# Performance work log

Hardware: AMD Instinct MI355X
Metric: run time of the kernel (lower is better)

Reference implementation:

```python
import jax, jax.numpy as jnp
import numpy as np
from jax import lax

POS_CANDIDATE = 128
SCL_TEMP = 0.1
BASE_SCL_TEMP = 0.07
N = 4096  # args.batch_size == total feature rows
D = 256
NUM_CLASSES = 8


def setup_inputs() -> dict:
    key = jax.random.key(0)
    k1, k2 = jax.random.split(key)
    features = jax.random.normal(k1, (N, D), dtype=jnp.float32)
    labels = jax.random.randint(k2, (N // 2,), 0, NUM_CLASSES, dtype=jnp.int64)
    return {"features": features, "labels": labels, "n_views": 1}


def reference(features, labels, n_views):
    n = features.shape[0]
    # labels path: mask_{ij} = 1 if same class
    lab = jnp.concatenate([labels, labels], axis=0).reshape(-1, 1)  # [N,1]
    mask = (lab == lab.T).astype(jnp.float32)                       # [N,N]

    # L2 normalize rows
    f = features / jnp.linalg.norm(features, axis=1, keepdims=True)

    # pairwise euclidean distances on detached features
    fd = lax.stop_gradient(f)
    sq = jnp.sum(fd * fd, axis=1)                                   # [N]
    d2 = sq[:, None] + sq[None, :] - 2.0 * (fd @ fd.T)
    dist = jnp.sqrt(jnp.maximum(d2, 0.0))                           # [N,N]

    # torch.topk default largest=True -> farthest POS_CANDIDATE indices
    _, pos_idx = lax.top_k(dist, POS_CANDIDATE)                     # [N,K]
    rows = jnp.arange(n)[:, None]
    dist_mask = jnp.zeros((n, n), jnp.float32).at[rows, pos_idx].set(1.0)

    # contrastive logits
    anchor_dot_contrast = (f @ f.T) / SCL_TEMP
    logits_max = jnp.max(anchor_dot_contrast, axis=1, keepdims=True)
    logits = anchor_dot_contrast - lax.stop_gradient(logits_max)

    # zero out self-contrast (arange scatter == zero diagonal, n_views=1)
    logits_mask = 1.0 - jnp.eye(n, dtype=jnp.float32)
    mask = mask * logits_mask

    exp_logits = jnp.exp(logits) * logits_mask
    log_prob = logits - jnp.log(jnp.sum(exp_logits, axis=1, keepdims=True))

    final_mask = mask * dist_mask
    mean_log_prob_pos = jnp.sum(final_mask * log_prob, axis=1) / jnp.sum(final_mask, axis=1)

    loss = -(SCL_TEMP / BASE_SCL_TEMP) * mean_log_prob_pos
    return jnp.mean(loss.reshape(n_views, n))
```

## Files before the change

### kernel.cpp

```cpp
#include <hip/hip_runtime.h>
#include <hip/hip_bf16.h>
#include <math.h>

#define NROWS 4096
#define DIM   256
#define HALF_MASK 2047
#define BLOCK 256

typedef __attribute__((ext_vector_type(8))) short bf16x8;
typedef __attribute__((ext_vector_type(4))) float f32x4;

__device__ __forceinline__ unsigned fkey(float f) {
    unsigned u = __float_as_uint(f);
    return (u & 0x80000000u) ? ~u : (u | 0x80000000u);
}

__device__ __forceinline__ unsigned qkey(float dot) {
    const float f = fmaf(dot, -2147483648.f, 2147483648.f);
    return (unsigned)fminf(fmaxf(f, 0.f), 4294967040.f);
}

__device__ __forceinline__ float bf16f(unsigned short b) {
    return __uint_as_float(((unsigned)b) << 16);
}


__global__ void prep_bf16_kernel(const float* __restrict__ feat,
                                 const int* __restrict__ labels,
                                 short* __restrict__ fnb,
                                 float* __restrict__ sq,
                                 unsigned char* __restrict__ lab8)
{
    const int row  = blockIdx.x * 4 + (threadIdx.x >> 6);
    const int lane = threadIdx.x & 63;
    float4 x = ((const float4*)feat)[(size_t)row * 64 + lane];
    float ss = x.x*x.x + x.y*x.y + x.z*x.z + x.w*x.w;
    #pragma unroll
    for (int m = 1; m < 64; m <<= 1) ss += __shfl_xor(ss, m, 64);
    const float nrm = sqrtf(ss);
    float4 f; f.x = x.x/nrm; f.y = x.y/nrm; f.z = x.z/nrm; f.w = x.w/nrm;

    union { __hip_bfloat16 b; unsigned short s; } cv[4];
    cv[0].b = __float2bfloat16(f.x); cv[1].b = __float2bfloat16(f.y);
    cv[2].b = __float2bfloat16(f.z); cv[3].b = __float2bfloat16(f.w);
    ushort4 h; h.x = cv[0].s; h.y = cv[1].s; h.z = cv[2].s; h.w = cv[3].s;
    ((ushort4*)fnb)[(size_t)row * 64 + lane] = h;

    float s2 = f.x*f.x + f.y*f.y + f.z*f.z + f.w*f.w;
    #pragma unroll
    for (int m = 1; m < 64; m <<= 1) s2 += __shfl_xor(s2, m, 64);
    if (lane == 0) {
        sq[row]   = s2;
        lab8[row] = (unsigned char)labels[row & HALF_MASK];
    }
}

__global__ __launch_bounds__(256) void gram_kernel(
        const short* __restrict__ fnb, unsigned short* __restrict__ Sb)
{
    __shared__ __align__(16) short As[128 * 64];
    __shared__ __align__(16) short Bs[128 * 64];

    const int tid  = threadIdx.x;
    const int lane = tid & 63;
    const int wv   = tid >> 6;
    const int wm   = wv >> 1, wn = wv & 1;
    const int wgid = (blockIdx.x & 7) * 128 + (blockIdx.x >> 3);
    const int bi   = wgid >> 5;
    const int bj   = wgid & 31;
    const int i0   = bi * 128, j0 = bj * 128;

    f32x4 acc[4][4];
    const f32x4 zero = {0.f, 0.f, 0.f, 0.f};
    #pragma unroll
    for (int a = 0; a < 4; ++a)
        #pragma unroll
        for (int b = 0; b < 4; ++b) acc[a][b] = zero;

    const int srow   = tid >> 3;
    const int schunk = tid & 7;

    for (int kt = 0; kt < 4; ++kt) {
        #pragma unroll
        for (int is = 0; is < 4; ++is) {
            const int row = is * 32 + srow;
            const size_t gsrc = (size_t)kt * 64 + schunk * 8;
            uint4 va = *(const uint4*)(fnb + (size_t)(i0 + row) * DIM + gsrc);
            uint4 vb = *(const uint4*)(fnb + (size_t)(j0 + row) * DIM + gsrc);
            const int dst = row * 64 + ((schunk ^ (row & 7)) * 8);
            *(uint4*)(As + dst) = va;
            *(uint4*)(Bs + dst) = vb;
        }
        __syncthreads();
        #pragma unroll
        for (int kk = 0; kk < 2; ++kk) {
            bf16x8 af[4], bfr[4];
            #pragma unroll
            for (int mi = 0; mi < 4; ++mi) {
                const int row = wm * 64 + mi * 16 + (lane & 15);
                const int ch  = kk * 4 + (lane >> 4);
                af[mi] = *(const bf16x8*)(As + row * 64 + ((ch ^ (row & 7)) * 8));
            }
            #pragma unroll
            for (int ni = 0; ni < 4; ++ni) {
                const int row = wn * 64 + ni * 16 + (lane & 15);
                const int ch  = kk * 4 + (lane >> 4);
                bfr[ni] = *(const bf16x8*)(Bs + row * 64 + ((ch ^ (row & 7)) * 8));
            }
            #pragma unroll
            for (int mi = 0; mi < 4; ++mi)
                #pragma unroll
                for (int ni = 0; ni < 4; ++ni)
                    acc[mi][ni] = __builtin_amdgcn_mfma_f32_16x16x32_bf16(
                        af[mi], bfr[ni], acc[mi][ni], 0, 0, 0);
        }
        __syncthreads();
    }

    const int cq = lane >> 4;
    const int cc = lane & 15;
    #pragma unroll
    for (int mi = 0; mi < 4; ++mi) {
        #pragma unroll
        for (int ni = 0; ni < 4; ++ni) {
            const int col  = j0 + wn * 64 + ni * 16 + cc;
            const int rowb = i0 + wm * 64 + mi * 16 + cq * 4;
            #pragma unroll
            for (int v = 0; v < 4; ++v) {
                union { __hip_bfloat16 b; unsigned short s; } cv;
                cv.b = __float2bfloat16(acc[mi][ni][v]);
                Sb[(size_t)(rowb + v) * NROWS + col] = cv.s;
            }
        }
    }
}

__device__ __forceinline__ void radix_scan(const unsigned* hb, int lane,
                                           unsigned& P, unsigned& K, int shift) {
    const uint4 h = ((const uint4*)hb)[lane];
    const unsigned s3 = h.w;
    const unsigned s2 = h.z + s3;
    const unsigned s1 = h.y + s2;
    const unsigned s0 = h.x + s1;
    unsigned x = s0;
    #pragma unroll
    for (int d = 1; d < 64; d <<= 1) {
        const unsigned y = __shfl_down(x, d, 64);
        if (lane + d < 64) x += y;
    }
    const unsigned E = x - s0;
    unsigned pk = 0u;
    const unsigned Sv0 = E + s0, Sv1 = E + s1, Sv2 = E + s2, Sv3 = E + s3;
    if (Sv0 >= K && Sv0 - h.x < K) pk = ((unsigned)(lane*4+0) << 16) | (K - (Sv0 - h.x));
    if (Sv1 >= K && Sv1 - h.y < K) pk = ((unsigned)(lane*4+1) << 16) | (K - (Sv1 - h.y));
    if (Sv2 >= K && Sv2 - h.z < K) pk = ((unsigned)(lane*4+2) << 16) | (K - (Sv2 - h.z));
    if (Sv3 >= K && Sv3 - h.w < K) pk = ((unsigned)(lane*4+3) << 16) | (K - (Sv3 - h.w));
    #pragma unroll
    for (int m = 1; m < 64; m <<= 1) pk |= __shfl_xor(pk, m, 64);
    P |= (pk >> 16) << shift;
    K  = pk & 0xFFFFu;
}

__global__ __launch_bounds__(256) void rowsel_b_kernel(
        const unsigned short* __restrict__ Sb,
        const unsigned char* __restrict__ lab8,
        float* __restrict__ partial)
{
    __shared__ unsigned hist[2][256];
    __shared__ float    zb[4];
    __shared__ unsigned tieb[4];
    __shared__ float    sdb[4];
    __shared__ int      cntb[4];

    const int tid  = threadIdx.x;
    const int lane = tid & 63;
    const int w    = tid >> 6;
    const int row  = blockIdx.x;

    hist[0][tid] = 0u;
    hist[1][tid] = 0u;
    __syncthreads();

    const uint4 s0 = ((const uint4*)(Sb + (size_t)row * NROWS))[tid * 2];
    const uint4 s1 = ((const uint4*)(Sb + (size_t)row * NROWS))[tid * 2 + 1];
    const uint4 lv = ((const uint4*)lab8)[tid];
    unsigned sw[8] = {s0.x, s0.y, s0.z, s0.w, s1.x, s1.y, s1.z, s1.w};
    const unsigned lw[4] = {lv.x, lv.y, lv.z, lv.w};

    unsigned q[16];
    float z = 0.f;
    const int j0 = tid * 16;
    #pragma unroll
    for (int e = 0; e < 16; ++e) {
        const unsigned word = sw[e >> 1];
        const float dot = bf16f((unsigned short)((e & 1) ? (word >> 16) : (word & 0xFFFFu)));
        q[e] = qkey(dot);
        z += (j0 + e == row) ? 0.f : __expf(10.f * dot);
        atomicAdd(&hist[0][q[e] >> 24], 1u);
    }
    #pragma unroll
    for (int m = 1; m < 64; m <<= 1) z += __shfl_xor(z, m, 64);
    if (lane == 0) zb[w] = z;
    __syncthreads();

    unsigned P = 0u, K = 128u;
    radix_scan(hist[0], lane, P, K, 24);

    #pragma unroll
    for (int e = 0; e < 16; ++e)
        if (((q[e] ^ P) >> 24) == 0u)
            atomicAdd(&hist[1][(q[e] >> 16) & 255u], 1u);
    __syncthreads();
    radix_scan(hist[1], lane, P, K, 16);
    hist[0][tid] = 0u;
    __syncthreads();

    #pragma unroll
    for (int e = 0; e < 16; ++e)
        if (((q[e] ^ P) >> 16) == 0u)
            atomicAdd(&hist[0][(q[e] >> 8) & 255u], 1u);
    __syncthreads();
    radix_scan(hist[0], lane, P, K, 8);
    const unsigned Ph = P >> 8;

    int tcnt = 0;
    #pragma unroll
    for (int e = 0; e < 16; ++e) tcnt += ((q[e] >> 8) == Ph) ? 1 : 0;
    int p = tcnt;
    #pragma unroll
    for (int d = 1; d < 64; d <<= 1) {
        const int o = __shfl_up(p, d, 64);
        if (lane >= d) p += o;
    }
    if (lane == 63) tieb[w] = (unsigned)p;
    __syncthreads();
    int t = p - tcnt;
    #pragma unroll
    for (int ww = 0; ww < 4; ++ww) if (ww < w) t += (int)tieb[ww];

    const unsigned my = lab8[row];
    float sd = 0.f; int cnt = 0;
    #pragma unroll
    for (int e = 0; e < 16; ++e) {
        const unsigned qh = q[e] >> 8;
        bool sel = (qh > Ph);
        if (qh == Ph) { sel = (t < (int)K); ++t; }
        const unsigned lj = (lw[e >> 2] >> ((e & 3) * 8)) & 255u;
        if (sel && (j0 + e != row) && lj == my) {
            ++cnt;
            sd += fmaf((float)q[e], -4.6566128730773926e-10f, 1.0f);
        }
    }
    #pragma unroll
    for (int m = 1; m < 64; m <<= 1) {
        sd  += __shfl_xor(sd, m, 64);
        cnt += __shfl_xor(cnt, m, 64);
    }
    if (lane == 0) { sdb[w] = sd; cntb[w] = cnt; }
    __syncthreads();

    if (tid == 0) {
        const int c = cntb[0] + cntb[1] + cntb[2] + cntb[3];
        float r = 0.f;
        if (c > 0) {
            const float s = sdb[0] + sdb[1] + sdb[2] + sdb[3];
            const float Z = zb[0] + zb[1] + zb[2] + zb[3];
            const float mlpp = (10.f * s) / (float)c - __logf(Z);
            r = -(0.1f / 0.07f) * mlpp * (1.f / (float)NROWS);
        }
        partial[row] = r;
    }
}

__global__ __launch_bounds__(256) void reduce_kernel(
        const float* __restrict__ partial, float* __restrict__ out)
{
    __shared__ float wsum[4];
    const int tid  = threadIdx.x;
    const int lane = tid & 63;
    const int w    = tid >> 6;
    float s = 0.f;
    #pragma unroll
    for (int k = 0; k < 4; ++k) {
        const float4 v = ((const float4*)partial)[tid + 256 * k];
        s += v.x + v.y + v.z + v.w;
    }
    #pragma unroll
    for (int m = 1; m < 64; m <<= 1) s += __shfl_xor(s, m, 64);
    if (lane == 0) wsum[w] = s;
    __syncthreads();
    if (tid == 0) out[0] = wsum[0] + wsum[1] + wsum[2] + wsum[3];
}


__global__ void prep_kernel(const float* __restrict__ feat,
                            const int* __restrict__ labels,
                            float* __restrict__ fn,
                            float* __restrict__ sq,
                            unsigned char* __restrict__ lab8,
                            float* __restrict__ out)
{
    const int row  = blockIdx.x * 4 + (threadIdx.x >> 6);
    const int lane = threadIdx.x & 63;
    float4 x = ((const float4*)feat)[(size_t)row * 64 + lane];
    float ss = x.x*x.x + x.y*x.y + x.z*x.z + x.w*x.w;
    #pragma unroll
    for (int m = 1; m < 64; m <<= 1) ss += __shfl_xor(ss, m, 64);
    const float nrm = sqrtf(ss);
    float4 f; f.x = x.x/nrm; f.y = x.y/nrm; f.z = x.z/nrm; f.w = x.w/nrm;
    ((float4*)fn)[(size_t)row * 64 + lane] = f;
    float s2 = f.x*f.x + f.y*f.y + f.z*f.z + f.w*f.w;
    #pragma unroll
    for (int m = 1; m < 64; m <<= 1) s2 += __shfl_xor(s2, m, 64);
    if (lane == 0) {
        sq[row]  = s2;
        lab8[row] = (unsigned char)labels[row & HALF_MASK];
    }
    if (blockIdx.x == 0 && threadIdx.x == 0) out[0] = 0.0f;
}

#define R 4
__global__ __launch_bounds__(BLOCK, 3) void rowloss_kernel(
        const float* __restrict__ fn,
        const float* __restrict__ sq,
        const unsigned char* __restrict__ lab8,
        float* __restrict__ out)
{
    __shared__ __align__(16) float fi[R][DIM];
    __shared__ unsigned hist[R * 256];
    __shared__ float    wz[R][4];
    __shared__ unsigned wsc[R][4];
    __shared__ unsigned selT[R], selK[R];
    __shared__ float    wsd[R][4];
    __shared__ int      wcnt[R][4];

    const int tid  = threadIdx.x;
    const int lane = tid & 63;
    const int wv   = tid >> 6;
    const int i0   = blockIdx.x * R;
    const int j0   = tid * 16;

    for (int idx = tid; idx < R * DIM; idx += BLOCK)
        fi[idx >> 8][idx & 255] = fn[(size_t)i0 * DIM + idx];
    __syncthreads();

    const float4* fn4 = (const float4*)fn;
    const float4* fi4 = (const float4*)&fi[0][0];

    float acc[16][R];
    #pragma unroll
    for (int jj = 0; jj < 16; ++jj)
        #pragma unroll
        for (int r = 0; r < R; ++r) acc[jj][r] = 0.0f;

    for (int c = 0; c < 32; ++c) {
        float fir[R][8];
        #pragma unroll
        for (int r = 0; r < R; ++r) {
            float4 a = fi4[r * 64 + c * 2];
            float4 b = fi4[r * 64 + c * 2 + 1];
            fir[r][0] = a.x; fir[r][1] = a.y; fir[r][2] = a.z; fir[r][3] = a.w;
            fir[r][4] = b.x; fir[r][5] = b.y; fir[r][6] = b.z; fir[r][7] = b.w;
        }
        #pragma unroll
        for (int jj = 0; jj < 16; ++jj) {
            const float4* pp = fn4 + (size_t)(j0 + jj) * 64 + c * 2;
            float4 x = pp[0];
            float4 y = pp[1];
            #pragma unroll
            for (int r = 0; r < R; ++r) {
                float s = acc[jj][r];
                s = fmaf(x.x, fir[r][0], s); s = fmaf(x.y, fir[r][1], s);
                s = fmaf(x.z, fir[r][2], s); s = fmaf(x.w, fir[r][3], s);
                s = fmaf(y.x, fir[r][4], s); s = fmaf(y.y, fir[r][5], s);
                s = fmaf(y.z, fir[r][6], s); s = fmaf(y.w, fir[r][7], s);
                acc[jj][r] = s;
            }
        }
    }

    float sqr[16];
    #pragma unroll
    for (int k = 0; k < 16; ++k) sqr[k] = sq[j0 + k];

    float lzr[R];
    {
        float zloc[R];
        #pragma unroll
        for (int r = 0; r < R; ++r) {
            const int ir = i0 + r;
            float z = 0.0f;
            #pragma unroll
            for (int k = 0; k < 16; ++k) {
                float e = __expf(10.0f * acc[k][r]);
                z += (j0 + k == ir) ? 0.0f : e;
            }
            zloc[r] = z;
        }
        #pragma unroll
        for (int r = 0; r < R; ++r) {
            float z = zloc[r];
            #pragma unroll
            for (int m = 1; m < 64; m <<= 1) z += __shfl_xor(z, m, 64);
            if (lane == 0) wz[r][wv] = z;
        }
        __syncthreads();
        #pragma unroll
        for (int r = 0; r < R; ++r)
            lzr[r] = __logf(wz[r][0] + wz[r][1] + wz[r][2] + wz[r][3]);
    }

    unsigned Pr[R] = {0, 0, 0, 0};
    unsigned Kr[R] = {128u, 128u, 128u, 128u};
    #pragma unroll
    for (int pass = 0; pass < 4; ++pass) {
        const int shift = 24 - 8 * pass;
        #pragma unroll
        for (int r = 0; r < R; ++r) hist[r * 256 + tid] = 0u;
        __syncthreads();
        #pragma unroll
        for (int r = 0; r < R; ++r) {
            #pragma unroll
            for (int k = 0; k < 16; ++k) {
                unsigned uu = fkey(fmaf(-2.0f, acc[k][r], sqr[k]));
                bool act = (pass == 0) ||
                    (((unsigned long long)(uu ^ Pr[r]) >> (shift + 8)) == 0ull);
                if (act) atomicAdd(&hist[r * 256 + ((uu >> shift) & 255u)], 1u);
            }
        }
        __syncthreads();
        unsigned g[R], Pv[R];
        #pragma unroll
        for (int r = 0; r < R; ++r) { g[r] = hist[r * 256 + (255 - tid)]; Pv[r] = g[r]; }
        #pragma unroll
        for (int dd = 1; dd < 64; dd <<= 1) {
            #pragma unroll
            for (int r = 0; r < R; ++r) {
                unsigned o = __shfl_up(Pv[r], dd, 64);
                if (lane >= dd) Pv[r] += o;
            }
        }
        if (lane == 63) {
            #pragma unroll
            for (int r = 0; r < R; ++r) wsc[r][wv] = Pv[r];
        }
        __syncthreads();
        #pragma unroll
        for (int r = 0; r < R; ++r) {
            unsigned off = 0;
            #pragma unroll
            for (int ww = 0; ww < 4; ++ww) if (ww < wv) off += wsc[r][ww];
            const unsigned Sv = Pv[r] + off;
            const unsigned Sn = Sv - g[r];
            if (Sv >= Kr[r] && Sn < Kr[r]) {
                selT[r] = Pr[r] | ((unsigned)(255 - tid) << shift);
                selK[r] = Kr[r] - Sn;
            }
        }
        __syncthreads();
        #pragma unroll
        for (int r = 0; r < R; ++r) { Pr[r] = selT[r]; Kr[r] = selK[r]; }
        __syncthreads();
    }

    int tb[R];
    {
        int tcr[R], Pt[R];
        #pragma unroll
        for (int r = 0; r < R; ++r) {
            int c = 0;
            #pragma unroll
            for (int k = 0; k < 16; ++k)
                if (fkey(fmaf(-2.0f, acc[k][r], sqr[k])) == Pr[r]) c++;
            tcr[r] = c; Pt[r] = c;
        }
        #pragma unroll
        for (int dd = 1; dd < 64; dd <<= 1) {
            #pragma unroll
            for (int r = 0; r < R; ++r) {
                int o = __shfl_up(Pt[r], dd, 64);
                if (lane >= dd) Pt[r] += o;
            }
        }
        if (lane == 63) {
            #pragma unroll
            for (int r = 0; r < R; ++r) wsc[r][wv] = (unsigned)Pt[r];
        }
        __syncthreads();
        #pragma unroll
        for (int r = 0; r < R; ++r) {
            int off = 0;
            #pragma unroll
            for (int ww = 0; ww < 4; ++ww) if (ww < wv) off += (int)wsc[r][ww];
            tb[r] = Pt[r] + off - tcr[r];
        }
    }

    const uint4 labv = ((const uint4*)lab8)[tid];
    const unsigned labw[4] = {labv.x, labv.y, labv.z, labv.w};

    #pragma unroll
    for (int r = 0; r < R; ++r) {
        const int ir = i0 + r;
        const unsigned my = lab8[ir];
        float sd = 0.0f; int cnt = 0; int t = tb[r];
        #pragma unroll
        for (int k = 0; k < 16; ++k) {
            const unsigned uu = fkey(fmaf(-2.0f, acc[k][r], sqr[k]));
            bool sel = (uu > Pr[r]);
            if (uu == Pr[r]) { sel = (t < (int)Kr[r]); t++; }
            const unsigned lj = (labw[k >> 2] >> ((k & 3) * 8)) & 255u;
            if (sel && (j0 + k != ir) && lj == my) { cnt++; sd += acc[k][r]; }
        }
        #pragma unroll
        for (int m = 1; m < 64; m <<= 1) {
            sd  += __shfl_xor(sd, m, 64);
            cnt += __shfl_xor(cnt, m, 64);
        }
        if (lane == 0) { wsd[r][wv] = sd; wcnt[r][wv] = cnt; }
    }
    __syncthreads();

    if (tid < R) {
        const int r = tid;
        const int c = wcnt[r][0] + wcnt[r][1] + wcnt[r][2] + wcnt[r][3];
        if (c > 0) {
            const float sd = wsd[r][0] + wsd[r][1] + wsd[r][2] + wsd[r][3];
            const float mlpp = (10.0f * sd) / (float)c - lzr[r];
            atomicAdd(out, -(0.1f / 0.07f) * mlpp * (1.0f / (float)NROWS));
        }
    }
}


extern "C" void kernel_launch(void* const* d_in, const int* in_sizes, int n_in,
                              void* d_out, int out_size, void* d_ws, size_t ws_size,
                              hipStream_t stream) {
    (void)in_sizes; (void)n_in; (void)out_size;
    const float* feat  = (const float*)d_in[0];
    const int* labels  = (const int*)d_in[1];
    float* out = (float*)d_out;

    const size_t offS = 0;
    const size_t offF = (size_t)NROWS * NROWS * 2;
    const size_t offQ = offF + (size_t)NROWS * DIM * 2;
    const size_t offL = offQ + (size_t)NROWS * 4;
    const size_t offP = offL + (size_t)NROWS;
    const size_t need = offP + (size_t)NROWS * 4;

    if (ws_size >= need) {
        unsigned short* Sb = (unsigned short*)((char*)d_ws + offS);
        short* fnb = (short*)((char*)d_ws + offF);
        float* sq  = (float*)((char*)d_ws + offQ);
        unsigned char* lab8 = (unsigned char*)((char*)d_ws + offL);
        float* partial = (float*)((char*)d_ws + offP);

        prep_bf16_kernel<<<NROWS / 4, BLOCK, 0, stream>>>(feat, labels, fnb, sq, lab8);
        gram_kernel<<<(NROWS / 128) * (NROWS / 128), BLOCK, 0, stream>>>(fnb, Sb);
        rowsel_b_kernel<<<NROWS, BLOCK, 0, stream>>>(Sb, lab8, partial);
        reduce_kernel<<<1, BLOCK, 0, stream>>>(partial, out);
    } else {
        float* fn = (float*)d_ws;
        float* sq = fn + (size_t)NROWS * DIM;
        unsigned char* lab8 = (unsigned char*)(sq + NROWS);

        prep_kernel<<<NROWS / 4, BLOCK, 0, stream>>>(feat, labels, fn, sq, lab8, out);
        rowloss_kernel<<<NROWS / R, BLOCK, 0, stream>>>(fn, sq, lab8, out);
    }
}
```

Measured before the change: 55.43 us.

## Shrink top-k radix key to 16 bits and stage gram output through LDS

The distance key is quantized to 16 bits instead of 32, so the radix select needs two histogram passes rather than three, which removes a histogram pass, a scan and several barriers per row. The selected-sum now reads the bf16 dot value directly instead of recovering it from the key. The gram kernel's epilogue writes its tile into swizzled shared memory and then stores 16-byte rows to global memory, replacing scattered 2-byte stores. The coarser key can change tie-breaking at the top-k boundary, which may alter which neighbours are selected.

```diff
diff --git a/kernel.cpp b/kernel.cpp
--- a/kernel.cpp
+++ b/kernel.cpp
@@ -15,9 +15,9 @@
     return (u & 0x80000000u) ? ~u : (u | 0x80000000u);
 }
 
-__device__ __forceinline__ unsigned qkey(float dot) {
-    const float f = fmaf(dot, -2147483648.f, 2147483648.f);
-    return (unsigned)fminf(fmaxf(f, 0.f), 4294967040.f);
+__device__ __forceinline__ unsigned qkey16(float dot) {
+    const float f = fmaf(dot, -16384.f, 16384.f);
+    return (unsigned)fminf(fmaxf(f, 0.f), 65535.f);
 }
 
 __device__ __forceinline__ float bf16f(unsigned short b) {
@@ -58,8 +58,9 @@
 __global__ __launch_bounds__(256) void gram_kernel(
         const short* __restrict__ fnb, unsigned short* __restrict__ Sb)
 {
-    __shared__ __align__(16) short As[128 * 64];
-    __shared__ __align__(16) short Bs[128 * 64];
+    __shared__ __align__(16) short smem[128 * 128];
+    short* As = smem;
+    short* Bs = smem + 128 * 64;
 
     const int tid  = threadIdx.x;
     const int lane = tid & 63;
@@ -123,15 +124,26 @@
     for (int mi = 0; mi < 4; ++mi) {
         #pragma unroll
         for (int ni = 0; ni < 4; ++ni) {
-            const int col  = j0 + wn * 64 + ni * 16 + cc;
-            const int rowb = i0 + wm * 64 + mi * 16 + cq * 4;
+            const int cl = wn * 64 + ni * 16 + cc;
+            const int rb = wm * 64 + mi * 16 + cq * 4;
             #pragma unroll
             for (int v = 0; v < 4; ++v) {
                 union { __hip_bfloat16 b; unsigned short s; } cv;
                 cv.b = __float2bfloat16(acc[mi][ni][v]);
-                Sb[(size_t)(rowb + v) * NROWS + col] = cv.s;
-            }
-        }
+                const int r = rb + v;
+                smem[r * 128 + (cl ^ (((unsigned)r & 7u) << 3))] = (short)cv.s;
+            }
+        }
+    }
+    __syncthreads();
+
+    #pragma unroll
+    for (int i = 0; i < 8; ++i) {
+        const int chunk = i * 256 + tid;
+        const int r     = chunk >> 4;
+        const int g     = (chunk & 15) ^ ((unsigned)r & 7u);
+        const uint4 val = *(const uint4*)(smem + r * 128 + g * 8);
+        *(uint4*)(Sb + (size_t)(i0 + r) * NROWS + j0 + ((chunk & 15) * 8)) = val;
     }
 }
 
@@ -194,9 +206,9 @@
     for (int e = 0; e < 16; ++e) {
         const unsigned word = sw[e >> 1];
         const float dot = bf16f((unsigned short)((e & 1) ? (word >> 16) : (word & 0xFFFFu)));
-        q[e] = qkey(dot);
+        q[e] = qkey16(dot);
         z += (j0 + e == row) ? 0.f : __expf(10.f * dot);
-        atomicAdd(&hist[0][q[e] >> 24], 1u);
+        atomicAdd(&hist[0][q[e] >> 8], 1u);
     }
     #pragma unroll
     for (int m = 1; m < 64; m <<= 1) z += __shfl_xor(z, m, 64);
@@ -204,28 +216,18 @@
     __syncthreads();
 
     unsigned P = 0u, K = 128u;
-    radix_scan(hist[0], lane, P, K, 24);
+    radix_scan(hist[0], lane, P, K, 8);
 
     #pragma unroll
     for (int e = 0; e < 16; ++e)
-        if (((q[e] ^ P) >> 24) == 0u)
-            atomicAdd(&hist[1][(q[e] >> 16) & 255u], 1u);
-    __syncthreads();
-    radix_scan(hist[1], lane, P, K, 16);
-    hist[0][tid] = 0u;
-    __syncthreads();
-
-    #pragma unroll
-    for (int e = 0; e < 16; ++e)
-        if (((q[e] ^ P) >> 16) == 0u)
-            atomicAdd(&hist[0][(q[e] >> 8) & 255u], 1u);
-    __syncthreads();
-    radix_scan(hist[0], lane, P, K, 8);
-    const unsigned Ph = P >> 8;
+        if ((q[e] >> 8) == (P >> 8))
+            atomicAdd(&hist[1][q[e] & 255u], 1u);
+    __syncthreads();
+    radix_scan(hist[1], lane, P, K, 0);
 
     int tcnt = 0;
     #pragma unroll
-    for (int e = 0; e < 16; ++e) tcnt += ((q[e] >> 8) == Ph) ? 1 : 0;
+    for (int e = 0; e < 16; ++e) tcnt += (q[e] == P) ? 1 : 0;
     int p = tcnt;
     #pragma unroll
     for (int d = 1; d < 64; d <<= 1) {
@@ -242,13 +244,13 @@
     float sd = 0.f; int cnt = 0;
     #pragma unroll
     for (int e = 0; e < 16; ++e) {
-        const unsigned qh = q[e] >> 8;
-        bool sel = (qh > Ph);
-        if (qh == Ph) { sel = (t < (int)K); ++t; }
+        bool sel = (q[e] > P);
+        if (q[e] == P) { sel = (t < (int)K); ++t; }
         const unsigned lj = (lw[e >> 2] >> ((e & 3) * 8)) & 255u;
         if (sel && (j0 + e != row) && lj == my) {
             ++cnt;
-            sd += fmaf((float)q[e], -4.6566128730773926e-10f, 1.0f);
+            const unsigned word = sw[e >> 1];
+            sd += bf16f((unsigned short)((e & 1) ? (word >> 16) : (word & 0xFFFFu)));
         }
     }
     #pragma unroll
```

Measured after the change: 53.84 us, median of 2. -2.9%, faster.
